# Kernel tuning notes

Measured on AMD Instinct MI355X. Metric: run time of the kernel, lower is better.

The kernel has to match this reference:

```python
import jax, jax.numpy as jnp
import numpy as np

VOCAB, EMB = 32000, 300
B, T, S = 64, 25, 50
NF = 100
FS = (3, 4, 5)
H = 256
OUT = 31


def setup_inputs() -> dict:
    key = jax.random.key(0)
    ks = jax.random.split(key, 12)
    inp = {}
    inp["dialogue"] = jax.random.randint(ks[0], (B, T, S), 0, VOCAB)
    inp["emb"] = jax.random.normal(ks[1], (VOCAB, EMB), jnp.float32) * 0.1
    for j, fs in enumerate(FS):
        inp[f"conv_w{fs}"] = jax.random.normal(ks[2 + j], (NF, 1, fs, EMB), jnp.float32) * (1.0 / np.sqrt(fs * EMB))
        inp[f"conv_b{fs}"] = jnp.zeros((NF,), jnp.float32)
    IN = NF * len(FS)
    sc = 1.0 / np.sqrt(H)
    inp["wih"] = jax.random.normal(ks[5], (4 * H, IN), jnp.float32) * sc
    inp["whh"] = jax.random.normal(ks[6], (4 * H, H), jnp.float32) * sc
    inp["bih"] = jnp.zeros((4 * H,), jnp.float32)
    inp["bhh"] = jnp.zeros((4 * H,), jnp.float32)
    inp["wih_r"] = jax.random.normal(ks[7], (4 * H, IN), jnp.float32) * sc
    inp["whh_r"] = jax.random.normal(ks[8], (4 * H, H), jnp.float32) * sc
    inp["bih_r"] = jnp.zeros((4 * H,), jnp.float32)
    inp["bhh_r"] = jnp.zeros((4 * H,), jnp.float32)
    inp["h2o_w"] = jax.random.normal(ks[9], (OUT, 2 * H), jnp.float32) * sc
    inp["h2o_b"] = jnp.zeros((OUT,), jnp.float32)
    return inp


def _cnn_embed(tokens, emb, conv_params):
    # tokens: [B,T,S] int -> per-utterance CNN features [B,T, NF*len(FS)]
    x = emb[tokens.reshape(-1, S)]           # [B*T, S, EMB] embedding lookup
    x = x[:, None, :, :]                      # NCHW: [B*T, 1, S, EMB]
    feats = []
    for (w, b) in conv_params:
        c = jax.lax.conv_general_dilated(
            x, w, (1, 1), 'VALID', dimension_numbers=('NCHW', 'OIHW', 'NCHW'))
        c = jax.nn.relu(c + b[None, :, None, None])   # [B*T, NF, S-fs+1, 1]
        feats.append(jnp.max(c[..., 0], axis=2))      # max-pool over time -> [B*T, NF]
    return jnp.concatenate(feats, axis=1).reshape(B, T, -1)


def _lstm(x, wih, whh, bih, bhh):
    # single-layer LSTM, torch gate order (i, f, g, o); x: [B,Tm,I] -> [B,Tm,H]
    h0 = jnp.zeros((x.shape[0], H), x.dtype)

    def step(carry, xt):
        h, c = carry
        g = xt @ wih.T + h @ whh.T + bih + bhh        # [B, 4H]
        i, f, gg, o = jnp.split(g, 4, axis=-1)
        c = jax.nn.sigmoid(f) * c + jax.nn.sigmoid(i) * jnp.tanh(gg)
        h = jax.nn.sigmoid(o) * jnp.tanh(c)
        return (h, c), h

    _, hs = jax.lax.scan(step, (h0, h0), jnp.swapaxes(x, 0, 1))
    return jnp.swapaxes(hs, 0, 1)


def reference(dialogue, emb, conv_w3, conv_b3, conv_w4, conv_b4, conv_w5, conv_b5,
              wih, whh, bih, bhh, wih_r, whh_r, bih_r, bhh_r, h2o_w, h2o_b):
    r_in = _cnn_embed(dialogue, emb,
                      [(conv_w3, conv_b3), (conv_w4, conv_b4), (conv_w5, conv_b5)])
    # bi=True branch: self.rnn consumes the sequence in reverse order, outputs
    # stored back at their original positions == reverse, scan, reverse.
    rev = _lstm(r_in[:, ::-1], wih, whh, bih, bhh)[:, ::-1]
    # rnn_r consumes the sequence forward (teacher_forcing_ratio=None path)
    fwd = _lstm(r_in, wih_r, whh_r, bih_r, bhh_r)
    h = jnp.concatenate([rev, fwd], axis=-1)          # [B,T,2H]
    return jax.nn.sigmoid(h @ h2o_w.T + h2o_b)        # [B,T,OUT]
```

## Files before the change

### kernel.cpp

```cpp
#include <hip/hip_runtime.h>
#include <hip/hip_bf16.h>

#define NB 64
#define NT 25
#define NS 50
#define EMBD 300
#define NFILT 100
#define HD 256
#define NOUT 31
#define NBT (NB*NT)

#define KP3 928
#define KP4 1216
#define KP5 1504
#define XS_LEN 15104

typedef __attribute__((ext_vector_type(8))) short short8;
typedef __attribute__((ext_vector_type(4))) float f32x4;

__device__ __forceinline__ float hsum4(float4 a) { return (a.x + a.y) + (a.z + a.w); }
__device__ __forceinline__ void fma4(float4& a, float4 w, float4 x) {
    a.x = fmaf(w.x, x.x, a.x); a.y = fmaf(w.y, x.y, a.y);
    a.z = fmaf(w.z, x.z, a.z); a.w = fmaf(w.w, x.w, a.w);
}
__device__ __forceinline__ float sigmoidf_(float x) { return 1.0f / (1.0f + __expf(-x)); }
__device__ __forceinline__ float tanh_fast(float x) {
    x = fminf(fmaxf(x, -15.0f), 15.0f);
    const float e = __expf(2.0f * x);
    return (e - 1.0f) / (e + 1.0f);
}

__device__ __forceinline__ unsigned short f2bf(float f) {
    union { float f; unsigned u; } v; v.f = f;
    unsigned r = v.u + 0x7FFF + ((v.u >> 16) & 1);
    return (unsigned short)(r >> 16);
}

__device__ __forceinline__ short8 ld8_a8(const unsigned short* p) {
    short8 r;
    ((uint2*)&r)[0] = *(const uint2*)p;
    ((uint2*)&r)[1] = *(const uint2*)(p + 4);
    return r;
}

__device__ __forceinline__ void gload_lds16(const unsigned short* g, unsigned short* l) {
    __builtin_amdgcn_global_load_lds(
        (const __attribute__((address_space(1))) unsigned int*)g,
        (__attribute__((address_space(3))) unsigned int*)l, 16, 0, 0);
}

__global__ __launch_bounds__(256) void k_prep(
    const float* __restrict__ w3, const float* __restrict__ w4, const float* __restrict__ w5,
    unsigned short* __restrict__ wb)
{
    const int S0 = 112 * KP3, S1 = S0 + 112 * KP4, S2 = S1 + 112 * KP5;
    int idx = blockIdx.x * 256 + threadIdx.x;
    if (idx >= S2) return;
    int rel, Kp, K; const float* src;
    if (idx < S0)      { rel = idx;      Kp = KP3; K = 900;  src = w3; }
    else if (idx < S1) { rel = idx - S0; Kp = KP4; K = 1200; src = w4; }
    else               { rel = idx - S1; Kp = KP5; K = 1500; src = w5; }
    int f = rel / Kp, k = rel - f * Kp;
    float v = (f < NFILT && k < K) ? src[(size_t)f * K + k] : 0.0f;
    wb[idx] = f2bf(v);
}

__global__ __launch_bounds__(256) void k_prep2(
    const float* __restrict__ whh, const float* __restrict__ whh_r,
    unsigned short* __restrict__ wb2)
{
    const int idx = blockIdx.x * 256 + threadIdx.x;
    const int dir = idx >> 18;
    const int rem = idx & 262143;
    const int n = rem >> 8, k = rem & 255;
    const int j = n >> 2, gate = n & 3;
    const float* src = dir ? whh_r : whh;
    const float v = src[(size_t)(gate * 256 + j) * 256 + k];
    const int w = n >> 7, r = n & 127;
    const int kk = k >> 5, kg = (k >> 3) & 3, e = k & 7;
    const size_t dst = ((size_t)(dir * 8 + w) * 8 + kk) * 4096
                     + r * 32 + ((kg ^ ((r >> 1) & 3)) * 8) + e;
    wb2[dst] = f2bf(v);
}

__global__ __launch_bounds__(512) void k_conv(
    const int* __restrict__ tok, const float* __restrict__ emb,
    const unsigned short* __restrict__ wb,
    const float* __restrict__ b3, const float* __restrict__ b4, const float* __restrict__ b5,
    float* __restrict__ rin)
{
    __shared__ unsigned short xs[2][XS_LEN];
    const int bt0 = blockIdx.x * 2;
    const int tid = threadIdx.x;
    for (int i4 = tid; i4 < 2 * NS * 75; i4 += 512) {
        const int smp = i4 / (NS * 75);
        const int rem = i4 - smp * (NS * 75);
        const int s = rem / 75, e4 = rem - s * 75;
        const int t = tok[(bt0 + smp) * NS + s];
        float4 v = ((const float4*)(emb + (size_t)t * EMBD))[e4];
        uint2 pk;
        pk.x = (unsigned)f2bf(v.x) | ((unsigned)f2bf(v.y) << 16);
        pk.y = (unsigned)f2bf(v.z) | ((unsigned)f2bf(v.w) << 16);
        *(uint2*)(&xs[smp][s * 300 + e4 * 4]) = pk;
    }
    for (int i = NS * EMBD + tid; i < XS_LEN; i += 512) { xs[0][i] = 0; xs[1][i] = 0; }
    __syncthreads();

    const int wave = tid >> 6, lane = tid & 63;
    const int col = lane & 15, kg = lane >> 4;

    for (int job = wave; job < 21; job += 8) {
        const int fsi = job / 7, ntile = job - fsi * 7;
        int Kp, P, obase; const unsigned short* W; const float* bias;
        if (fsi == 0)      { Kp = KP3; P = 48; W = wb;                       bias = b3; obase = 0; }
        else if (fsi == 1) { Kp = KP4; P = 47; W = wb + 112 * KP3;           bias = b4; obase = NFILT; }
        else               { Kp = KP5; P = 46; W = wb + 112 * (KP3 + KP4);   bias = b5; obase = 2 * NFILT; }

        const unsigned short* wrow = W + (size_t)(ntile * 16 + col) * Kp + kg * 8;
        const unsigned short* xb0 = &xs[0][col * 300 + kg * 8];
        const unsigned short* xb1 = &xs[1][col * 300 + kg * 8];
        f32x4 a00 = {0,0,0,0}, a01 = {0,0,0,0}, a02 = {0,0,0,0};
        f32x4 a10 = {0,0,0,0}, a11 = {0,0,0,0}, a12 = {0,0,0,0};

        const int nks = Kp / 32;
        short8 wr0 = *(const short8*)(wrow);
        short8 wr1 = *(const short8*)(wrow + 32);
        for (int ks = 0; ks < nks; ++ks) {
            const int k0 = ks * 32;
            short8 bfrag = wr0;
            wr0 = wr1;
            if (ks + 2 < nks) wr1 = *(const short8*)(wrow + k0 + 64);
            short8 p0 = ld8_a8(xb0 + k0);
            short8 p1 = ld8_a8(xb0 + 16 * 300 + k0);
            short8 p2 = ld8_a8(xb0 + 32 * 300 + k0);
            short8 q0 = ld8_a8(xb1 + k0);
            short8 q1 = ld8_a8(xb1 + 16 * 300 + k0);
            short8 q2 = ld8_a8(xb1 + 32 * 300 + k0);
            a00 = __builtin_amdgcn_mfma_f32_16x16x32_bf16(p0, bfrag, a00, 0, 0, 0);
            a01 = __builtin_amdgcn_mfma_f32_16x16x32_bf16(p1, bfrag, a01, 0, 0, 0);
            a02 = __builtin_amdgcn_mfma_f32_16x16x32_bf16(p2, bfrag, a02, 0, 0, 0);
            a10 = __builtin_amdgcn_mfma_f32_16x16x32_bf16(q0, bfrag, a10, 0, 0, 0);
            a11 = __builtin_amdgcn_mfma_f32_16x16x32_bf16(q1, bfrag, a11, 0, 0, 0);
            a12 = __builtin_amdgcn_mfma_f32_16x16x32_bf16(q2, bfrag, a12, 0, 0, 0);
        }

        float pm0 = -1e30f, pm1 = -1e30f;
        #pragma unroll
        for (int reg = 0; reg < 4; ++reg) {
            pm0 = fmaxf(pm0, a00[reg]); pm0 = fmaxf(pm0, a01[reg]);
            pm1 = fmaxf(pm1, a10[reg]); pm1 = fmaxf(pm1, a11[reg]);
            const int r2 = 32 + kg * 4 + reg;
            if (r2 < P) { pm0 = fmaxf(pm0, a02[reg]); pm1 = fmaxf(pm1, a12[reg]); }
        }
        pm0 = fmaxf(pm0, __shfl_xor(pm0, 16, 64));
        pm0 = fmaxf(pm0, __shfl_xor(pm0, 32, 64));
        pm1 = fmaxf(pm1, __shfl_xor(pm1, 16, 64));
        pm1 = fmaxf(pm1, __shfl_xor(pm1, 32, 64));
        if (lane < 16) {
            const int f = ntile * 16 + lane;
            if (f < NFILT) {
                const float bb = bias[f];
                rin[(size_t)bt0 * (3 * NFILT) + obase + f]       = fmaxf(0.0f, pm0 + bb);
                rin[(size_t)(bt0 + 1) * (3 * NFILT) + obase + f] = fmaxf(0.0f, pm1 + bb);
            }
        }
    }
}

__global__ __launch_bounds__(256) void k_gin(
    const float* __restrict__ rin,
    const float* __restrict__ wih,   const float* __restrict__ bih,   const float* __restrict__ bhh,
    const float* __restrict__ wih_r, const float* __restrict__ bih_r, const float* __restrict__ bhh_r,
    float* __restrict__ gin)
{
    __shared__ float xsh[8 * EMBD];
    const int bt0 = blockIdx.x * 8;
    const int tid = threadIdx.x;
    const float4* src = (const float4*)(rin + (size_t)bt0 * EMBD);
    for (int i4 = tid; i4 < 8 * EMBD / 4; i4 += 256) ((float4*)xsh)[i4] = src[i4];
    __syncthreads();
    for (int g2 = tid; g2 < 2 * 1024; g2 += 256) {
        const int d = g2 >> 10;
        const int g = g2 & 1023;
        const float* wp = (d ? wih_r : wih) + (size_t)g * EMBD;
        const float bb = d ? (bih_r[g] + bhh_r[g]) : (bih[g] + bhh[g]);
        const float4* w4p = (const float4*)wp;
        float4 acc[8];
        #pragma unroll
        for (int r = 0; r < 8; ++r) acc[r] = {0,0,0,0};
        for (int k = 0; k < EMBD / 4; ++k) {
            const float4 wv = w4p[k];
            #pragma unroll
            for (int r = 0; r < 8; ++r) fma4(acc[r], wv, ((const float4*)(xsh + r * EMBD))[k]);
        }
        const int gp = ((g & 255) << 2) | (g >> 8);
        #pragma unroll
        for (int r = 0; r < 8; ++r) {
            const int bt = bt0 + r;
            const int b = bt / NT, t = bt - b * NT;
            gin[(((size_t)d * NT + t) * NB + b) * 1024 + gp] = hsum4(acc[r]) + bb;
        }
    }
}

__global__ __launch_bounds__(512, 1) void k_lstm(
    const float* __restrict__ gin,
    const unsigned short* __restrict__ wb2,
    float* __restrict__ hs)
{
    const int bid = blockIdx.x;
    const int dir = bid >> 2, bq = bid & 3;
    const int tid = threadIdx.x;
    const int wave = tid >> 6, lane = tid & 63;
    const int l15 = lane & 15, kg = lane >> 4;
    const int m = l15 & 3, quad = l15 >> 2;

    __shared__ __align__(16) unsigned short wring[8][2][4096];
    __shared__ __align__(16) unsigned short hb[2][16 * 264];

    for (int i = tid; i < 16 * 264; i += 512) hb[0][i] = 0;
    __syncthreads();

    const unsigned short* wsrc = wb2 + ((size_t)(dir * 8 + wave) * 8) * 4096;
    unsigned short* wd0 = &wring[wave][0][0];
    unsigned short* wd1 = &wring[wave][1][0];

    const float* gb = gin + (size_t)dir * (NT * NB * 1024);
    float* hsb = hs + (size_t)dir * NBT * HD;

    const int b_row = kg * 4 + m;
    const int bglob = bq * 16 + b_row;

    float c[8] = {0.f,0.f,0.f,0.f,0.f,0.f,0.f,0.f};

    for (int s = 0; s < NT; ++s) {
        const int t = dir ? s : (NT - 1 - s);
        const unsigned short* hc = hb[s & 1];
        unsigned short* hn = hb[(s + 1) & 1];

        float4 gxr[8];
        #pragma unroll
        for (int nt = 0; nt < 8; ++nt) {
            const int j_g = wave * 32 + nt * 4 + quad;
            gxr[nt] = *(const float4*)(gb + (((size_t)t * NB + bglob) << 10) + j_g * 4);
        }
        #pragma unroll
        for (int i = 0; i < 8; ++i) gload_lds16(wsrc + i * 512 + lane * 8, wd0 + i * 512);
        #pragma unroll
        for (int i = 0; i < 8; ++i) gload_lds16(wsrc + 4096 + i * 512 + lane * 8, wd1 + i * 512);

        f32x4 acc[8];
        #pragma unroll
        for (int nt = 0; nt < 8; ++nt) acc[nt] = (f32x4){0.f, 0.f, 0.f, 0.f};

        #pragma unroll
        for (int kk = 0; kk < 8; ++kk) {
            if (kk < 7) asm volatile("s_waitcnt vmcnt(8)" ::: "memory");
            else        asm volatile("s_waitcnt vmcnt(0)" ::: "memory");
            __builtin_amdgcn_sched_barrier(0);
            const unsigned short* wt = (kk & 1) ? wd1 : wd0;
            const short8 av = *(const short8*)(hc + l15 * 264 + kk * 32 + kg * 8);
            #pragma unroll
            for (int nt = 0; nt < 8; ++nt) {
                const int row = nt * 16 + l15;
                const short8 bbf = *(const short8*)(wt + row * 32 + ((kg ^ ((row >> 1) & 3)) * 8));
                acc[nt] = __builtin_amdgcn_mfma_f32_16x16x32_bf16(av, bbf, acc[nt], 0, 0, 0);
            }
            if (kk + 2 < 8) {
                asm volatile("s_waitcnt lgkmcnt(0)" ::: "memory");
                unsigned short* wref = (kk & 1) ? wd1 : wd0;
                #pragma unroll
                for (int i = 0; i < 8; ++i)
                    gload_lds16(wsrc + (kk + 2) * 4096 + i * 512 + lane * 8, wref + i * 512);
            }
        }

        #pragma unroll
        for (int nt = 0; nt < 8; ++nt) {
            float r0 = acc[nt][0], r1 = acc[nt][1], r2 = acc[nt][2], r3 = acc[nt][3];
            { float x = (m & 1) ? r0 : r1; x = __shfl_xor(x, 1, 64); if (m & 1) r0 = x; else r1 = x; }
            { float x = (m & 1) ? r2 : r3; x = __shfl_xor(x, 1, 64); if (m & 1) r2 = x; else r3 = x; }
            { float x = (m & 2) ? r0 : r2; x = __shfl_xor(x, 2, 64); if (m & 2) r0 = x; else r2 = x; }
            { float x = (m & 2) ? r1 : r3; x = __shfl_xor(x, 2, 64); if (m & 2) r1 = x; else r3 = x; }
            const float4 gx = gxr[nt];
            const float vi = sigmoidf_(r0 + gx.x);
            const float vf = sigmoidf_(r1 + gx.y);
            const float vg = tanh_fast(r2 + gx.z);
            const float vo = sigmoidf_(r3 + gx.w);
            const float cc = vf * c[nt] + vi * vg;
            c[nt] = cc;
            const float hh = vo * tanh_fast(cc);
            const int j_g = wave * 32 + nt * 4 + quad;
            hn[b_row * 264 + j_g] = f2bf(hh);
            hsb[((size_t)bglob * NT + t) * HD + j_g] = hh;
        }
        __syncthreads();
    }
}

__global__ __launch_bounds__(64) void k_out(
    const float* __restrict__ hs, const float* __restrict__ w, const float* __restrict__ bias,
    float* __restrict__ out)
{
    __shared__ float hsh[2 * HD];
    const int bt = blockIdx.x;
    const int tid = threadIdx.x;
    const float4* rev4 = (const float4*)(hs + (size_t)bt * HD);
    const float4* fwd4 = (const float4*)(hs + ((size_t)NBT + bt) * HD);
    for (int i = tid; i < 2 * HD / 4; i += 64)
        ((float4*)hsh)[i] = (i < HD / 4) ? rev4[i] : fwd4[i - HD / 4];
    __syncthreads();
    if (tid < NOUT) {
        const float4* wr = (const float4*)(w + (size_t)tid * (2 * HD));
        float4 acc{0,0,0,0};
        for (int k = 0; k < 2 * HD / 4; ++k) fma4(acc, wr[k], ((const float4*)hsh)[k]);
        out[(size_t)bt * NOUT + tid] = sigmoidf_(hsum4(acc) + bias[tid]);
    }
}

extern "C" void kernel_launch(void* const* d_in, const int* in_sizes, int n_in,
                              void* d_out, int out_size, void* d_ws, size_t ws_size,
                              hipStream_t stream)
{
    const int*   tok   = (const int*)d_in[0];
    const float* emb   = (const float*)d_in[1];
    const float* w3    = (const float*)d_in[2];
    const float* b3    = (const float*)d_in[3];
    const float* w4    = (const float*)d_in[4];
    const float* b4    = (const float*)d_in[5];
    const float* w5    = (const float*)d_in[6];
    const float* b5    = (const float*)d_in[7];
    const float* wih   = (const float*)d_in[8];
    const float* whh   = (const float*)d_in[9];
    const float* bih   = (const float*)d_in[10];
    const float* bhh   = (const float*)d_in[11];
    const float* wih_r = (const float*)d_in[12];
    const float* whh_r = (const float*)d_in[13];
    const float* bih_r = (const float*)d_in[14];
    const float* bhh_r = (const float*)d_in[15];
    const float* h2o_w = (const float*)d_in[16];
    const float* h2o_b = (const float*)d_in[17];

    float* ws  = (float*)d_ws;
    float* rin = ws;
    float* gin = rin + (size_t)NBT * 3 * NFILT;
    float* hs  = gin + (size_t)2 * NBT * 1024;
    unsigned short* wb  = (unsigned short*)gin;
    unsigned short* wb2 = (unsigned short*)rin;

    k_prep <<<1596, 256, 0, stream>>>(w3, w4, w5, wb);
    k_conv <<<NBT / 2, 512, 0, stream>>>(tok, emb, wb, b3, b4, b5, rin);
    k_gin  <<<NBT / 8, 256, 0, stream>>>(rin, wih, bih, bhh, wih_r, bih_r, bhh_r, gin);
    k_prep2<<<2048, 256, 0, stream>>>(whh, whh_r, wb2);
    k_lstm <<<8, 512, 0, stream>>>(gin, wb2, hs);
    k_out  <<<NBT, 64, 0, stream>>>(hs, h2o_w, h2o_b, (float*)d_out);
}
```

Before: 478.0 us.

## Stream LSTM recurrent weights into registers and stage gate inputs via LDS

The recurrent LSTM kernel drops from 8 to 4 waves per block, each wave owning 64 hidden units. The bf16 Whh tiles are repacked so each lane loads its MFMA B operand straight into registers with global_load_dwordx4, replacing the LDS ring buffer and its lgkmcnt waits. Gate pre-activations are brought into LDS with async global_load_lds instead of per-thread float4 loads. This trades more VGPRs (two 16-register weight sets plus 16 accumulators) and fewer waves for removing an LDS round-trip on the latency-bound serial time loop.

```diff
diff --git a/kernel.cpp b/kernel.cpp
--- a/kernel.cpp
+++ b/kernel.cpp
@@ -17,6 +17,7 @@
 
 typedef __attribute__((ext_vector_type(8))) short short8;
 typedef __attribute__((ext_vector_type(4))) float f32x4;
+typedef __attribute__((ext_vector_type(4))) unsigned int u32x4;
 
 __device__ __forceinline__ float hsum4(float4 a) { return (a.x + a.y) + (a.z + a.w); }
 __device__ __forceinline__ void fma4(float4& a, float4 w, float4 x) {
@@ -43,10 +44,17 @@
     return r;
 }
 
-__device__ __forceinline__ void gload_lds16(const unsigned short* g, unsigned short* l) {
+__device__ __forceinline__ void gload_lds16f(const float* g, float* l) {
     __builtin_amdgcn_global_load_lds(
         (const __attribute__((address_space(1))) unsigned int*)g,
         (__attribute__((address_space(3))) unsigned int*)l, 16, 0, 0);
+}
+
+__device__ __forceinline__ void gld16(u32x4& d, const void* p) {
+    asm volatile("global_load_dwordx4 %0, %1, off" : "=v"(d) : "v"(p) : "memory");
+}
+__device__ __forceinline__ short8 as_bf16x8(u32x4 v) {
+    union { u32x4 u; short8 s; } c; c.u = v; return c.s;
 }
 
 __global__ __launch_bounds__(256) void k_prep(
@@ -76,10 +84,10 @@
     const int j = n >> 2, gate = n & 3;
     const float* src = dir ? whh_r : whh;
     const float v = src[(size_t)(gate * 256 + j) * 256 + k];
-    const int w = n >> 7, r = n & 127;
+    const int w4 = n >> 8, nt = (n >> 4) & 15, l15 = n & 15;
     const int kk = k >> 5, kg = (k >> 3) & 3, e = k & 7;
-    const size_t dst = ((size_t)(dir * 8 + w) * 8 + kk) * 4096
-                     + r * 32 + ((kg ^ ((r >> 1) & 3)) * 8) + e;
+    const size_t dst = ((size_t)(dir * 4 + w4) * 8 + kk) * 8192
+                     + nt * 512 + (kg * 16 + l15) * 8 + e;
     wb2[dst] = f2bf(v);
 }
 
@@ -203,7 +211,7 @@
     }
 }
 
-__global__ __launch_bounds__(512, 1) void k_lstm(
+__global__ __launch_bounds__(256, 1) void k_lstm(
     const float* __restrict__ gin,
     const unsigned short* __restrict__ wb2,
     float* __restrict__ hs)
@@ -211,78 +219,83 @@
     const int bid = blockIdx.x;
     const int dir = bid >> 2, bq = bid & 3;
     const int tid = threadIdx.x;
-    const int wave = tid >> 6, lane = tid & 63;
+    const int w4 = tid >> 6, lane = tid & 63;
     const int l15 = lane & 15, kg = lane >> 4;
     const int m = l15 & 3, quad = l15 >> 2;
 
-    __shared__ __align__(16) unsigned short wring[8][2][4096];
     __shared__ __align__(16) unsigned short hb[2][16 * 264];
-
-    for (int i = tid; i < 16 * 264; i += 512) hb[0][i] = 0;
+    __shared__ __align__(16) float gl[4][16 * 260];
+
+    for (int i = tid; i < 16 * 264; i += 256) hb[0][i] = 0;
     __syncthreads();
 
-    const unsigned short* wsrc = wb2 + ((size_t)(dir * 8 + wave) * 8) * 4096;
-    unsigned short* wd0 = &wring[wave][0][0];
-    unsigned short* wd1 = &wring[wave][1][0];
-
+    const unsigned short* wbase = wb2 + (size_t)(dir * 4 + w4) * 65536;
     const float* gb = gin + (size_t)dir * (NT * NB * 1024);
     float* hsb = hs + (size_t)dir * NBT * HD;
 
     const int b_row = kg * 4 + m;
     const int bglob = bq * 16 + b_row;
 
-    float c[8] = {0.f,0.f,0.f,0.f,0.f,0.f,0.f,0.f};
+    float c[16];
+    #pragma unroll
+    for (int q = 0; q < 16; ++q) c[q] = 0.0f;
 
     for (int s = 0; s < NT; ++s) {
         const int t = dir ? s : (NT - 1 - s);
         const unsigned short* hc = hb[s & 1];
         unsigned short* hn = hb[(s + 1) & 1];
 
-        float4 gxr[8];
-        #pragma unroll
-        for (int nt = 0; nt < 8; ++nt) {
-            const int j_g = wave * 32 + nt * 4 + quad;
-            gxr[nt] = *(const float4*)(gb + (((size_t)t * NB + bglob) << 10) + j_g * 4);
-        }
-        #pragma unroll
-        for (int i = 0; i < 8; ++i) gload_lds16(wsrc + i * 512 + lane * 8, wd0 + i * 512);
-        #pragma unroll
-        for (int i = 0; i < 8; ++i) gload_lds16(wsrc + 4096 + i * 512 + lane * 8, wd1 + i * 512);
-
-        f32x4 acc[8];
-        #pragma unroll
-        for (int nt = 0; nt < 8; ++nt) acc[nt] = (f32x4){0.f, 0.f, 0.f, 0.f};
+        float* gld = &gl[w4][0];
+        #pragma unroll
+        for (int b = 0; b < 16; ++b)
+            gload_lds16f(gb + (((size_t)t * NB + bq * 16 + b) << 10) + w4 * 256 + lane * 4,
+                         gld + b * 260);
+
+        u32x4 wA[16], wB[16];
+        #pragma unroll
+        for (int nt = 0; nt < 16; ++nt) gld16(wA[nt], wbase + nt * 512 + lane * 8);
+        #pragma unroll
+        for (int nt = 0; nt < 16; ++nt) gld16(wB[nt], wbase + 8192 + nt * 512 + lane * 8);
+
+        f32x4 acc[16];
+        #pragma unroll
+        for (int nt = 0; nt < 16; ++nt) acc[nt] = (f32x4){0.f, 0.f, 0.f, 0.f};
 
         #pragma unroll
         for (int kk = 0; kk < 8; ++kk) {
-            if (kk < 7) asm volatile("s_waitcnt vmcnt(8)" ::: "memory");
+            if (kk < 7) asm volatile("s_waitcnt vmcnt(16)" ::: "memory");
             else        asm volatile("s_waitcnt vmcnt(0)" ::: "memory");
             __builtin_amdgcn_sched_barrier(0);
-            const unsigned short* wt = (kk & 1) ? wd1 : wd0;
             const short8 av = *(const short8*)(hc + l15 * 264 + kk * 32 + kg * 8);
-            #pragma unroll
-            for (int nt = 0; nt < 8; ++nt) {
-                const int row = nt * 16 + l15;
-                const short8 bbf = *(const short8*)(wt + row * 32 + ((kg ^ ((row >> 1) & 3)) * 8));
-                acc[nt] = __builtin_amdgcn_mfma_f32_16x16x32_bf16(av, bbf, acc[nt], 0, 0, 0);
+            if ((kk & 1) == 0) {
+                #pragma unroll
+                for (int nt = 0; nt < 16; ++nt)
+                    acc[nt] = __builtin_amdgcn_mfma_f32_16x16x32_bf16(av, as_bf16x8(wA[nt]), acc[nt], 0, 0, 0);
+                if (kk + 2 < 8) {
+                    #pragma unroll
+                    for (int nt = 0; nt < 16; ++nt)
+                        gld16(wA[nt], wbase + (size_t)(kk + 2) * 8192 + nt * 512 + lane * 8);
+                }
+            } else {
+                #pragma unroll
+                for (int nt = 0; nt < 16; ++nt)
+                    acc[nt] = __builtin_amdgcn_mfma_f32_16x16x32_bf16(av, as_bf16x8(wB[nt]), acc[nt], 0, 0, 0);
+                if (kk + 2 < 8) {
+                    #pragma unroll
+                    for (int nt = 0; nt < 16; ++nt)
+                        gld16(wB[nt], wbase + (size_t)(kk + 2) * 8192 + nt * 512 + lane * 8);
+                }
             }
-            if (kk + 2 < 8) {
-                asm volatile("s_waitcnt lgkmcnt(0)" ::: "memory");
-                unsigned short* wref = (kk & 1) ? wd1 : wd0;
-                #pragma unroll
-                for (int i = 0; i < 8; ++i)
-                    gload_lds16(wsrc + (kk + 2) * 4096 + i * 512 + lane * 8, wref + i * 512);
-            }
-        }
-
-        #pragma unroll
-        for (int nt = 0; nt < 8; ++nt) {
+        }
+
+        #pragma unroll
+        for (int nt = 0; nt < 16; ++nt) {
             float r0 = acc[nt][0], r1 = acc[nt][1], r2 = acc[nt][2], r3 = acc[nt][3];
             { float x = (m & 1) ? r0 : r1; x = __shfl_xor(x, 1, 64); if (m & 1) r0 = x; else r1 = x; }
             { float x = (m & 1) ? r2 : r3; x = __shfl_xor(x, 1, 64); if (m & 1) r2 = x; else r3 = x; }
             { float x = (m & 2) ? r0 : r2; x = __shfl_xor(x, 2, 64); if (m & 2) r0 = x; else r2 = x; }
             { float x = (m & 2) ? r1 : r3; x = __shfl_xor(x, 2, 64); if (m & 2) r1 = x; else r3 = x; }
-            const float4 gx = gxr[nt];
+            const float4 gx = *(const float4*)(&gl[w4][b_row * 260 + (nt * 4 + quad) * 4]);
             const float vi = sigmoidf_(r0 + gx.x);
             const float vf = sigmoidf_(r1 + gx.y);
             const float vg = tanh_fast(r2 + gx.z);
@@ -290,7 +303,7 @@
             const float cc = vf * c[nt] + vi * vg;
             c[nt] = cc;
             const float hh = vo * tanh_fast(cc);
-            const int j_g = wave * 32 + nt * 4 + quad;
+            const int j_g = w4 * 64 + nt * 4 + quad;
             hn[b_row * 264 + j_g] = f2bf(hh);
             hsb[((size_t)bglob * NT + t) * HD + j_g] = hh;
         }
@@ -352,6 +365,6 @@
     k_conv <<<NBT / 2, 512, 0, stream>>>(tok, emb, wb, b3, b4, b5, rin);
     k_gin  <<<NBT / 8, 256, 0, stream>>>(rin, wih, bih, bhh, wih_r, bih_r, bhh_r, gin);
     k_prep2<<<2048, 256, 0, stream>>>(whh, whh_r, wb2);
-    k_lstm <<<8, 512, 0, stream>>>(gin, wb2, hs);
+    k_lstm <<<8, 256, 0, stream>>>(gin, wb2, hs);
     k_out  <<<NBT, 64, 0, stream>>>(hs, h2o_w, h2o_b, (float*)d_out);
 }
```

After: 502.1 us. 5.0% more time.

## Keep half of LSTM recurrent weights in registers, stream other half

Applied to the files above, without the earlier changes.

The recurrent weight matrix is re-laid out so each wave holds the first four n-tiles of W_hh in VGPRs for the whole sequence. Only the remaining four tiles are streamed from global memory into a smaller LDS ring each timestep. This halves per-step weight traffic on the serial LSTM critical path and drops the LDS swizzle addressing, at the cost of 128 extra VGPRs per lane and possible register pressure or spills.

```diff
diff --git a/kernel.cpp b/kernel.cpp
--- a/kernel.cpp
+++ b/kernel.cpp
@@ -15,6 +15,7 @@
 #define KP5 1504
 #define XS_LEN 15104
 
+typedef unsigned short ush;
 typedef __attribute__((ext_vector_type(8))) short short8;
 typedef __attribute__((ext_vector_type(4))) float f32x4;
 
@@ -30,20 +31,20 @@
     return (e - 1.0f) / (e + 1.0f);
 }
 
-__device__ __forceinline__ unsigned short f2bf(float f) {
+__device__ __forceinline__ ush f2bf(float f) {
     union { float f; unsigned u; } v; v.f = f;
     unsigned r = v.u + 0x7FFF + ((v.u >> 16) & 1);
-    return (unsigned short)(r >> 16);
-}
-
-__device__ __forceinline__ short8 ld8_a8(const unsigned short* p) {
+    return (ush)(r >> 16);
+}
+
+__device__ __forceinline__ short8 ld8_a8(const ush* p) {
     short8 r;
     ((uint2*)&r)[0] = *(const uint2*)p;
     ((uint2*)&r)[1] = *(const uint2*)(p + 4);
     return r;
 }
 
-__device__ __forceinline__ void gload_lds16(const unsigned short* g, unsigned short* l) {
+__device__ __forceinline__ void gload_lds16u(const ush* g, ush* l) {
     __builtin_amdgcn_global_load_lds(
         (const __attribute__((address_space(1))) unsigned int*)g,
         (__attribute__((address_space(3))) unsigned int*)l, 16, 0, 0);
@@ -51,7 +52,7 @@
 
 __global__ __launch_bounds__(256) void k_prep(
     const float* __restrict__ w3, const float* __restrict__ w4, const float* __restrict__ w5,
-    unsigned short* __restrict__ wb)
+    ush* __restrict__ wb)
 {
     const int S0 = 112 * KP3, S1 = S0 + 112 * KP4, S2 = S1 + 112 * KP5;
     int idx = blockIdx.x * 256 + threadIdx.x;
@@ -67,7 +68,7 @@
 
 __global__ __launch_bounds__(256) void k_prep2(
     const float* __restrict__ whh, const float* __restrict__ whh_r,
-    unsigned short* __restrict__ wb2)
+    ush* __restrict__ wb2)
 {
     const int idx = blockIdx.x * 256 + threadIdx.x;
     const int dir = idx >> 18;
@@ -77,19 +78,22 @@
     const float* src = dir ? whh_r : whh;
     const float v = src[(size_t)(gate * 256 + j) * 256 + k];
     const int w = n >> 7, r = n & 127;
+    const int nt = r >> 4, l15 = r & 15;
     const int kk = k >> 5, kg = (k >> 3) & 3, e = k & 7;
-    const size_t dst = ((size_t)(dir * 8 + w) * 8 + kk) * 4096
-                     + r * 32 + ((kg ^ ((r >> 1) & 3)) * 8) + e;
+    const int lane8 = (kg * 16 + l15) * 8 + e;
+    size_t dst = (size_t)(dir * 8 + w) * 32768;
+    if (nt < 4) dst += nt * 4096 + kk * 512 + lane8;
+    else        dst += 16384 + kk * 2048 + (nt - 4) * 512 + lane8;
     wb2[dst] = f2bf(v);
 }
 
 __global__ __launch_bounds__(512) void k_conv(
     const int* __restrict__ tok, const float* __restrict__ emb,
-    const unsigned short* __restrict__ wb,
+    const ush* __restrict__ wb,
     const float* __restrict__ b3, const float* __restrict__ b4, const float* __restrict__ b5,
     float* __restrict__ rin)
 {
-    __shared__ unsigned short xs[2][XS_LEN];
+    __shared__ ush xs[2][XS_LEN];
     const int bt0 = blockIdx.x * 2;
     const int tid = threadIdx.x;
     for (int i4 = tid; i4 < 2 * NS * 75; i4 += 512) {
@@ -111,14 +115,14 @@
 
     for (int job = wave; job < 21; job += 8) {
         const int fsi = job / 7, ntile = job - fsi * 7;
-        int Kp, P, obase; const unsigned short* W; const float* bias;
+        int Kp, P, obase; const ush* W; const float* bias;
         if (fsi == 0)      { Kp = KP3; P = 48; W = wb;                       bias = b3; obase = 0; }
         else if (fsi == 1) { Kp = KP4; P = 47; W = wb + 112 * KP3;           bias = b4; obase = NFILT; }
         else               { Kp = KP5; P = 46; W = wb + 112 * (KP3 + KP4);   bias = b5; obase = 2 * NFILT; }
 
-        const unsigned short* wrow = W + (size_t)(ntile * 16 + col) * Kp + kg * 8;
-        const unsigned short* xb0 = &xs[0][col * 300 + kg * 8];
-        const unsigned short* xb1 = &xs[1][col * 300 + kg * 8];
+        const ush* wrow = W + (size_t)(ntile * 16 + col) * Kp + kg * 8;
+        const ush* xb0 = &xs[0][col * 300 + kg * 8];
+        const ush* xb1 = &xs[1][col * 300 + kg * 8];
         f32x4 a00 = {0,0,0,0}, a01 = {0,0,0,0}, a02 = {0,0,0,0};
         f32x4 a10 = {0,0,0,0}, a11 = {0,0,0,0}, a12 = {0,0,0,0};
 
@@ -205,7 +209,7 @@
 
 __global__ __launch_bounds__(512, 1) void k_lstm(
     const float* __restrict__ gin,
-    const unsigned short* __restrict__ wb2,
+    const ush* __restrict__ wb2,
     float* __restrict__ hs)
 {
     const int bid = blockIdx.x;
@@ -215,19 +219,24 @@
     const int l15 = lane & 15, kg = lane >> 4;
     const int m = l15 & 3, quad = l15 >> 2;
 
-    __shared__ __align__(16) unsigned short wring[8][2][4096];
-    __shared__ __align__(16) unsigned short hb[2][16 * 264];
+    __shared__ __align__(16) ush hb[2][16 * 264];
+    __shared__ __align__(16) ush wring[8][2][2048];
 
     for (int i = tid; i < 16 * 264; i += 512) hb[0][i] = 0;
-    __syncthreads();
-
-    const unsigned short* wsrc = wb2 + ((size_t)(dir * 8 + wave) * 8) * 4096;
-    unsigned short* wd0 = &wring[wave][0][0];
-    unsigned short* wd1 = &wring[wave][1][0];
-
+
+    const ush* wbase = wb2 + (size_t)(dir * 8 + wave) * 32768;
+    const ush* wstr = wbase + 16384;
     const float* gb = gin + (size_t)dir * (NT * NB * 1024);
     float* hsb = hs + (size_t)dir * NBT * HD;
 
+    short8 wpa[4][8];
+    #pragma unroll
+    for (int nt = 0; nt < 4; ++nt)
+        #pragma unroll
+        for (int kk = 0; kk < 8; ++kk)
+            wpa[nt][kk] = *(const short8*)(wbase + nt * 4096 + kk * 512 + lane * 8);
+    __syncthreads();
+
     const int b_row = kg * 4 + m;
     const int bglob = bq * 16 + b_row;
 
@@ -235,8 +244,8 @@
 
     for (int s = 0; s < NT; ++s) {
         const int t = dir ? s : (NT - 1 - s);
-        const unsigned short* hc = hb[s & 1];
-        unsigned short* hn = hb[(s + 1) & 1];
+        const ush* hc = hb[s & 1];
+        ush* hn = hb[(s + 1) & 1];
 
         float4 gxr[8];
         #pragma unroll
@@ -244,10 +253,13 @@
             const int j_g = wave * 32 + nt * 4 + quad;
             gxr[nt] = *(const float4*)(gb + (((size_t)t * NB + bglob) << 10) + j_g * 4);
         }
-        #pragma unroll
-        for (int i = 0; i < 8; ++i) gload_lds16(wsrc + i * 512 + lane * 8, wd0 + i * 512);
-        #pragma unroll
-        for (int i = 0; i < 8; ++i) gload_lds16(wsrc + 4096 + i * 512 + lane * 8, wd1 + i * 512);
+
+        #pragma unroll
+        for (int q = 0; q < 4; ++q)
+            gload_lds16u(wstr + 0 * 2048 + q * 512 + lane * 8, &wring[wave][0][q * 512]);
+        #pragma unroll
+        for (int q = 0; q < 4; ++q)
+            gload_lds16u(wstr + 1 * 2048 + q * 512 + lane * 8, &wring[wave][1][q * 512]);
 
         f32x4 acc[8];
         #pragma unroll
@@ -255,23 +267,25 @@
 
         #pragma unroll
         for (int kk = 0; kk < 8; ++kk) {
-            if (kk < 7) asm volatile("s_waitcnt vmcnt(8)" ::: "memory");
+            if (kk < 7) asm volatile("s_waitcnt vmcnt(4)" ::: "memory");
             else        asm volatile("s_waitcnt vmcnt(0)" ::: "memory");
             __builtin_amdgcn_sched_barrier(0);
-            const unsigned short* wt = (kk & 1) ? wd1 : wd0;
             const short8 av = *(const short8*)(hc + l15 * 264 + kk * 32 + kg * 8);
             #pragma unroll
-            for (int nt = 0; nt < 8; ++nt) {
-                const int row = nt * 16 + l15;
-                const short8 bbf = *(const short8*)(wt + row * 32 + ((kg ^ ((row >> 1) & 3)) * 8));
-                acc[nt] = __builtin_amdgcn_mfma_f32_16x16x32_bf16(av, bbf, acc[nt], 0, 0, 0);
+            for (int nt = 0; nt < 4; ++nt)
+                acc[nt] = __builtin_amdgcn_mfma_f32_16x16x32_bf16(av, wpa[nt][kk], acc[nt], 0, 0, 0);
+            #pragma unroll
+            for (int q = 0; q < 4; ++q) {
+                const short8 bbf = *(const short8*)(&wring[wave][kk & 1][q * 512 + lane * 8]);
+                acc[4 + q] = __builtin_amdgcn_mfma_f32_16x16x32_bf16(av, bbf, acc[4 + q], 0, 0, 0);
             }
-            if (kk + 2 < 8) {
+            if (kk < 6) {
                 asm volatile("s_waitcnt lgkmcnt(0)" ::: "memory");
-                unsigned short* wref = (kk & 1) ? wd1 : wd0;
+                __builtin_amdgcn_sched_barrier(0);
                 #pragma unroll
-                for (int i = 0; i < 8; ++i)
-                    gload_lds16(wsrc + (kk + 2) * 4096 + i * 512 + lane * 8, wref + i * 512);
+                for (int q = 0; q < 4; ++q)
+                    gload_lds16u(wstr + (size_t)(kk + 2) * 2048 + q * 512 + lane * 8,
+                                 &wring[wave][kk & 1][q * 512]);
             }
         }
 
@@ -345,8 +359,8 @@
     float* rin = ws;
     float* gin = rin + (size_t)NBT * 3 * NFILT;
     float* hs  = gin + (size_t)2 * NBT * 1024;
-    unsigned short* wb  = (unsigned short*)gin;
-    unsigned short* wb2 = (unsigned short*)rin;
+    ush* wb  = (ush*)gin;
+    ush* wb2 = (ush*)rin;
 
     k_prep <<<1596, 256, 0, stream>>>(w3, w4, w5, wb);
     k_conv <<<NBT / 2, 512, 0, stream>>>(tok, emb, wb, b3, b4, b5, rin);
```

New measurement: 485.6 us. About the same (+1.6%).
